# Optimization experiments

Measured on AMD Instinct MI355X. Metric: run time of the kernel, lower is better.

Reference implementation:

```python
import jax, jax.numpy as jnp
import numpy as np

B, N, DIM, H, DH = 4, 2048, 512, 8, 64  # patches_num == N (required by the math)
INNER = H * DH
SCALE = DH ** -0.5


def setup_inputs() -> dict:
    key = jax.random.key(0)
    ks = jax.random.split(key, 6)
    s = lambda fan_in: 1.0 / np.sqrt(fan_in)
    return {
        "x": jax.random.normal(ks[0], (B, N, DIM), dtype=jnp.float32),
        "w_qkfv": jax.random.normal(ks[1], (DIM, 4 * INNER), dtype=jnp.float32) * s(DIM),
        "w_scales": jax.random.normal(ks[2], (DH, N), dtype=jnp.float32) * s(DH),
        "b_scales": jax.random.normal(ks[3], (N,), dtype=jnp.float32) * s(DH),
        "w_out": jax.random.normal(ks[4], (INNER, DIM), dtype=jnp.float32) * s(INNER),
        "b_out": jax.random.normal(ks[5], (DIM,), dtype=jnp.float32) * s(INNER),
    }


def reference(x, w_qkfv, w_scales, b_scales, w_out, b_out):
    # Fused qkfv projection: [B,N,4*INNER]
    qkfv = x @ w_qkfv
    q, k, f, v = jnp.split(qkfv, 4, axis=-1)
    split_heads = lambda t: t.reshape(B, N, H, DH).transpose(0, 2, 1, 3)  # b h n d
    q, k, f, v = map(split_heads, (q, k, f, v))

    # q @ k^T * scale -> [b,h,n,n]
    scores = jnp.einsum("bhid,bhjd->bhij", q, k) * SCALE
    attn = jax.nn.softmax(scores, axis=-1)

    # f^T @ v -> [b,h,d,d], then Linear(dim_head -> patches_num) -> [b,h,d,n]
    poss_value = jnp.einsum("bhnd,bhne->bhde", f, v)
    poss_value = poss_value @ w_scales + b_scales  # [b,h,d,n]

    # attn @ poss_value^T -> [b,h,n,d]
    out = jnp.einsum("bhij,bhdj->bhid", attn, poss_value)
    out = out.transpose(0, 2, 1, 3).reshape(B, N, INNER)  # b n (h d)

    # to_out (dropout=0 / eval mode -> identity)
    return out @ w_out + b_out
```

## Files before the change

### kernel.cpp

```cpp
#include <hip/hip_runtime.h>
#include <stdint.h>

#define N_SEQ 2048
#define QKFV_COLS 2048

typedef __attribute__((ext_vector_type(8))) __bf16 bf16x8;
typedef __attribute__((ext_vector_type(4))) __bf16 bf16x4;
typedef __attribute__((ext_vector_type(4))) float f32x4;
typedef __attribute__((ext_vector_type(16))) float f32x16;

#if __has_builtin(__builtin_amdgcn_exp2f)
#define EXP2(x) __builtin_amdgcn_exp2f(x)
#else
#define EXP2(x) exp2f(x)
#endif

__device__ __forceinline__ f32x4 mfma16(bf16x8 a, bf16x8 b, f32x4 c) {
  return __builtin_amdgcn_mfma_f32_16x16x32_bf16(a, b, c, 0, 0, 0);
}
__device__ __forceinline__ f32x16 mfma32(bf16x8 a, bf16x8 b, f32x16 c) {
  return __builtin_amdgcn_mfma_f32_32x32x16_bf16(a, b, c, 0, 0, 0);
}

__device__ __forceinline__ void glds16(const void* g, void* l) {
  __builtin_amdgcn_global_load_lds(
      (__attribute__((address_space(1))) uint32_t*)(uintptr_t)g,
      (__attribute__((address_space(3))) uint32_t*)l, 16, 0, 0);
}

__global__ __launch_bounds__(256) void prep_kernel(const float* __restrict__ wqk,
                                                   __bf16* __restrict__ wqT,
                                                   const float* __restrict__ wo,
                                                   __bf16* __restrict__ woT,
                                                   const float* __restrict__ wsc,
                                                   __bf16* __restrict__ wscT) {
  const int t = threadIdx.x;
  int bid = blockIdx.x;
  const float* in;
  __bf16* outp;
  int R, C, rt, ct;
  if (bid < 256) { in = wqk; outp = wqT; R = 512; C = 2048; rt = bid >> 5; ct = bid & 31; }
  else if (bid < 320) { int b2 = bid - 256; in = wo; outp = woT; R = 512; C = 512; rt = b2 >> 3; ct = b2 & 7; }
  else { int b2 = bid - 320; in = wsc; outp = wscT; R = 64; C = 2048; rt = 0; ct = b2; }
  __shared__ __bf16 tile[64][72];
  const int r0 = rt * 64, c0 = ct * 64;
  {
    const int r = t >> 2, cq = (t & 3) * 16;
    const float* src = in + (size_t)(r0 + r) * C + c0 + cq;
#pragma unroll
    for (int q = 0; q < 4; ++q) {
      f32x4 v = *(const f32x4*)(src + q * 4);
#pragma unroll
      for (int e = 0; e < 4; ++e) tile[r][cq + q * 4 + e] = (__bf16)v[e];
    }
  }
  __syncthreads();
  {
    const int c = t >> 2, rq = (t & 3) * 16;
    __bf16* dst = outp + (size_t)(c0 + c) * R + r0 + rq;
    bf16x8 o0, o1;
#pragma unroll
    for (int j = 0; j < 8; ++j) { o0[j] = tile[rq + j][c]; o1[j] = tile[rq + 8 + j][c]; }
    *(bf16x8*)dst = o0;
    *(bf16x8*)(dst + 8) = o1;
  }
}

__global__ __launch_bounds__(512, 4) void gemm_qkfv_kernel(const float* __restrict__ X,
                                                           const __bf16* __restrict__ Bt,
                                                           __bf16* __restrict__ C,
                                                           __bf16* __restrict__ fT,
                                                           __bf16* __restrict__ vT) {
  __shared__ alignas(16) __bf16 Ab[2][128 * 32];
  __shared__ alignas(16) __bf16 Bb[2][256 * 32];
  const int K = 512, N = 2048;
  const int t = threadIdx.x;
  const int w = t >> 6;
  const int lane = t & 63;
  const int l15 = lane & 15;
  const int q4 = lane >> 4;
  const int g4 = q4 * 4;
  const int wr = w >> 2, wc = w & 3;
  const int bid = blockIdx.x;
  const int n0 = (bid & 7) * 256;
  const int m0 = (bid >> 3) * 128;

  const float* srcAf;
  {
    int r = t >> 2, u = (t & 3) ^ (r & 3);
    srcAf = X + (size_t)(m0 + r) * K + u * 8;
  }
  const __bf16* srcB[2];
#pragma unroll
  for (int c = 0; c < 2; ++c) {
    int s = c * 512 + t, r = s >> 2, u = (s & 3) ^ (r & 3);
    srcB[c] = Bt + (size_t)(n0 + r) * K + u * 8;
  }

  f32x4 acc[4][4];
#pragma unroll
  for (int m = 0; m < 4; ++m)
#pragma unroll
    for (int n = 0; n < 4; ++n) acc[m][n] = (f32x4){0.f, 0.f, 0.f, 0.f};

  {
    f32x4 a0 = *(const f32x4*)(srcAf);
    f32x4 a1 = *(const f32x4*)(srcAf + 4);
    glds16(srcB[0], &Bb[0][t * 8]);
    glds16(srcB[1], &Bb[0][(512 + t) * 8]);
    bf16x8 aw;
#pragma unroll
    for (int e = 0; e < 4; ++e) { aw[e] = (__bf16)a0[e]; aw[4 + e] = (__bf16)a1[e]; }
    *(bf16x8*)&Ab[0][t * 8] = aw;
  }

  for (int kt = 0; kt < 16; ++kt) {
    const int cur = kt & 1;
    asm volatile("s_waitcnt vmcnt(0) lgkmcnt(0)" ::: "memory");
    __builtin_amdgcn_s_barrier();
    f32x4 a0, a1;
    const bool pf = kt < 15;
    if (pf) {
      const int k0 = (kt + 1) * 32;
      a0 = *(const f32x4*)(srcAf + k0);
      a1 = *(const f32x4*)(srcAf + k0 + 4);
      glds16(srcB[0] + k0, &Bb[cur ^ 1][t * 8]);
      glds16(srcB[1] + k0, &Bb[cur ^ 1][(512 + t) * 8]);
    }
    bf16x8 af[4], bf[4];
#pragma unroll
    for (int m = 0; m < 4; ++m) {
      const int R = wr * 64 + m * 16 + l15;
      af[m] = *(const bf16x8*)&Ab[cur][R * 32 + ((q4 ^ (R & 3)) * 8)];
    }
#pragma unroll
    for (int n = 0; n < 4; ++n) {
      const int R = wc * 64 + n * 16 + l15;
      bf[n] = *(const bf16x8*)&Bb[cur][R * 32 + ((q4 ^ (R & 3)) * 8)];
    }
    __builtin_amdgcn_s_setprio(1);
#pragma unroll
    for (int m = 0; m < 4; ++m)
#pragma unroll
      for (int n = 0; n < 4; ++n) acc[m][n] = mfma16(af[m], bf[n], acc[m][n]);
    __builtin_amdgcn_s_setprio(0);
    if (pf) {
      bf16x8 aw;
#pragma unroll
      for (int e = 0; e < 4; ++e) { aw[e] = (__bf16)a0[e]; aw[4 + e] = (__bf16)a1[e]; }
      *(bf16x8*)&Ab[cur ^ 1][t * 8] = aw;
    }
    __builtin_amdgcn_s_barrier();
  }

  if (n0 < 1024) {
#pragma unroll
    for (int m = 0; m < 4; ++m)
#pragma unroll
      for (int n = 0; n < 4; ++n) {
        const int col = n0 + wc * 64 + n * 16 + l15;
        const int row = m0 + wr * 64 + m * 16 + g4;
#pragma unroll
        for (int r = 0; r < 4; ++r)
          C[(size_t)(row + r) * N + col] = (__bf16)acc[m][n][r];
      }
  } else {
    __bf16* T = (n0 < 1536) ? fT : vT;
    const int cbase = (n0 < 1536) ? 1024 : 1536;
#pragma unroll
    for (int m = 0; m < 4; ++m)
#pragma unroll
      for (int n = 0; n < 4; ++n) {
        const int hc = n0 + wc * 64 + n * 16 + l15 - cbase;
        const int h = hc >> 6, d = hc & 63;
        const int row = m0 + wr * 64 + m * 16 + g4;
        const int b = row >> 11, nl = row & 2047;
        bf16x4 pk;
#pragma unroll
        for (int r = 0; r < 4; ++r) pk[r] = (__bf16)acc[m][n][r];
        *(bf16x4*)&T[(size_t)((b * 8 + h) * 64 + d) * 2048 + nl] = pk;
      }
  }
}

__global__ __launch_bounds__(512, 4) void gemm_out_kernel(const __bf16* __restrict__ A,
                                                          const __bf16* __restrict__ Bt,
                                                          float* __restrict__ out,
                                                          const float* __restrict__ bias) {
  __shared__ alignas(16) __bf16 Ab[2][128 * 32];
  __shared__ alignas(16) __bf16 Bb[2][64 * 32];
  const int K = 512, N = 512;
  const int t = threadIdx.x;
  const int w = t >> 6;
  const int lane = t & 63;
  const int l15 = lane & 15;
  const int q4 = lane >> 4;
  const int g4 = q4 * 4;
  const int wr = w >> 1, wc = w & 1;
  const int bid = blockIdx.x;
  const int m0 = (((bid & 7) | (((bid >> 3) & 7) << 3))) * 128;
  const int n0 = (bid >> 6) * 64;

  const __bf16* srcA;
  const __bf16* srcB;
  {
    int s = t, r = s >> 2, u = (s & 3) ^ (r & 3);
    srcA = A + (size_t)(m0 + r) * K + u * 8;
    srcB = Bt + (size_t)(n0 + (r & 63)) * K + u * 8;
  }

  f32x4 acc[2][2];
#pragma unroll
  for (int m = 0; m < 2; ++m)
#pragma unroll
    for (int n = 0; n < 2; ++n) acc[m][n] = (f32x4){0.f, 0.f, 0.f, 0.f};

  glds16(srcA, &Ab[0][t * 8]);
  if (t < 256) glds16(srcB, &Bb[0][t * 8]);

  for (int kt = 0; kt < 16; ++kt) {
    const int cur = kt & 1;
    asm volatile("s_waitcnt vmcnt(0)" ::: "memory");
    __builtin_amdgcn_s_barrier();
    if (kt < 15) {
      const int k0 = (kt + 1) * 32;
      glds16(srcA + k0, &Ab[cur ^ 1][t * 8]);
      if (t < 256) glds16(srcB + k0, &Bb[cur ^ 1][t * 8]);
    }
    bf16x8 af[2], bf[2];
#pragma unroll
    for (int m = 0; m < 2; ++m) {
      const int R = wr * 32 + m * 16 + l15;
      af[m] = *(const bf16x8*)&Ab[cur][R * 32 + ((q4 ^ (R & 3)) * 8)];
    }
#pragma unroll
    for (int n = 0; n < 2; ++n) {
      const int R = wc * 32 + n * 16 + l15;
      bf[n] = *(const bf16x8*)&Bb[cur][R * 32 + ((q4 ^ (R & 3)) * 8)];
    }
    __builtin_amdgcn_s_setprio(1);
#pragma unroll
    for (int m = 0; m < 2; ++m)
#pragma unroll
      for (int n = 0; n < 2; ++n) acc[m][n] = mfma16(af[m], bf[n], acc[m][n]);
    __builtin_amdgcn_s_setprio(0);
    __builtin_amdgcn_s_barrier();
  }

#pragma unroll
  for (int m = 0; m < 2; ++m)
#pragma unroll
    for (int n = 0; n < 2; ++n) {
      const int col = n0 + wc * 32 + n * 16 + l15;
      const float bv = bias[col];
      const int row = m0 + wr * 32 + m * 16 + g4;
#pragma unroll
      for (int r = 0; r < 4; ++r)
        out[(size_t)(row + r) * N + col] = acc[m][n][r] + bv;
    }
}

__global__ __launch_bounds__(256) void fvmm_kernel(const __bf16* __restrict__ fT,
                                                   const __bf16* __restrict__ vT,
                                                   float* __restrict__ fvp) {
  __shared__ alignas(16) __bf16 As[2 * 8192];
  __shared__ alignas(16) __bf16 Bs[2 * 8192];
  const int t = threadIdx.x;
  const int w = t >> 6;
  const int lane = t & 63;
  const int l15 = lane & 15;
  const int q4 = lane >> 4;
  const int g4 = q4 * 4;
  const int sl = blockIdx.x;
  const int bh = blockIdx.y;
  const int k0 = sl * 256;
  const __bf16* A = fT + (size_t)bh * 131072 + k0;
  const __bf16* B = vT + (size_t)bh * 131072 + k0;

#pragma unroll
  for (int kt = 0; kt < 2; ++kt)
#pragma unroll
    for (int c = 0; c < 4; ++c) {
      int slot = c * 256 + t;
      int r = slot >> 4, u = (slot & 15) ^ (r & 7);
      glds16(A + (size_t)r * 2048 + kt * 128 + u * 8, &As[kt * 8192 + (c * 256 + w * 64) * 8]);
      glds16(B + (size_t)r * 2048 + kt * 128 + u * 8, &Bs[kt * 8192 + (c * 256 + w * 64) * 8]);
    }
  asm volatile("s_waitcnt vmcnt(0)" ::: "memory");
  __syncthreads();

  f32x4 acc[4];
#pragma unroll
  for (int nb = 0; nb < 4; ++nb) acc[nb] = (f32x4){0.f, 0.f, 0.f, 0.f};
  const int arow = w * 16 + l15;
#pragma unroll
  for (int ks = 0; ks < 8; ++ks) {
    const int kt = ks >> 2;
    const int ku = (ks & 3) * 4 + q4;
    bf16x8 a = *(const bf16x8*)&As[kt * 8192 + arow * 128 + ((ku ^ (arow & 7)) * 8)];
#pragma unroll
    for (int nb = 0; nb < 4; ++nb) {
      const int br = nb * 16 + l15;
      bf16x8 bb = *(const bf16x8*)&Bs[kt * 8192 + br * 128 + ((ku ^ (br & 7)) * 8)];
      acc[nb] = mfma16(a, bb, acc[nb]);
    }
  }
  float* dst = fvp + (size_t)(sl * 32 + bh) * 4096;
#pragma unroll
  for (int nb = 0; nb < 4; ++nb)
#pragma unroll
    for (int r = 0; r < 4; ++r)
      dst[(w * 16 + g4 + r) * 64 + nb * 16 + l15] = acc[nb][r];
}

__global__ __launch_bounds__(256) void pvmat2_kernel(const float* __restrict__ fvp,
                                                     const __bf16* __restrict__ wscT,
                                                     const float* __restrict__ bsc,
                                                     __bf16* __restrict__ pvm) {
  __shared__ alignas(16) __bf16 fs[64 * 72];
  __shared__ alignas(16) __bf16 Ws[128 * 64];
  const int t = threadIdx.x;
  const int w = t >> 6;
  const int lane = t & 63;
  const int l15 = lane & 15;
  const int q4 = lane >> 4;
  const int g4 = q4 * 4;
  const int bh = blockIdx.y;
  const int j0 = blockIdx.x * 128;

#pragma unroll
  for (int c = 0; c < 4; ++c) {
    int slot = c * 256 + t;
    int r = slot >> 3, u = (slot & 7) ^ (r & 7);
    glds16(wscT + (size_t)(j0 + r) * 64 + u * 8, &Ws[(c * 256 + w * 64) * 8]);
  }
#pragma unroll
  for (int qq = 0; qq < 4; ++qq) {
    int idx = t * 16 + qq * 4;
    f32x4 s = (f32x4){0.f, 0.f, 0.f, 0.f};
#pragma unroll
    for (int sl = 0; sl < 8; ++sl)
      s += *(const f32x4*)&fvp[(size_t)(sl * 32 + bh) * 4096 + idx];
    bf16x4 pk;
#pragma unroll
    for (int e = 0; e < 4; ++e) pk[e] = (__bf16)s[e];
    *(bf16x4*)&fs[(idx >> 6) * 72 + (idx & 63)] = pk;
  }
  asm volatile("s_waitcnt vmcnt(0)" ::: "memory");
  __syncthreads();

  f32x4 acc[8];
#pragma unroll
  for (int nb = 0; nb < 8; ++nb) {
    float bv = bsc[j0 + nb * 16 + l15];
    acc[nb] = (f32x4){bv, bv, bv, bv};
  }
  const int arow = w * 16 + l15;
#pragma unroll
  for (int ks = 0; ks < 2; ++ks) {
    bf16x8 a = *(const bf16x8*)&fs[arow * 72 + ks * 32 + q4 * 8];
#pragma unroll
    for (int nb = 0; nb < 8; ++nb) {
      const int jr = nb * 16 + l15;
      bf16x8 bb = *(const bf16x8*)&Ws[jr * 64 + (((ks * 4 + q4) ^ (jr & 7)) * 8)];
      acc[nb] = mfma16(a, bb, acc[nb]);
    }
  }
  __bf16* dst = pvm + (size_t)bh * 131072 + (size_t)j0;
#pragma unroll
  for (int nb = 0; nb < 8; ++nb)
#pragma unroll
    for (int r = 0; r < 4; ++r)
      dst[(size_t)(w * 16 + g4 + r) * 2048 + nb * 16 + l15] = (__bf16)acc[nb][r];
}

__global__ __launch_bounds__(512, 4) void attn_kernel(const __bf16* __restrict__ qkfv,
                                                      const __bf16* __restrict__ pvm,
                                                      __bf16* __restrict__ obuf) {
  __shared__ alignas(16) char smem[65536];
  __bf16* Kb = (__bf16*)smem;
  __bf16* Vb = (__bf16*)(smem + 32768);
  const int t = threadIdx.x;
  const int w = t >> 6;
  const int g = w >> 2;
  const int wq = w & 3;
  const int lane = t & 63;
  const int ln = lane & 31;
  const int hi = lane >> 5;
  const int p = blockIdx.x;
  const int bh = (p & 7) * 4 + ((p >> 3) & 3);
  const int iblk = p >> 5;
  const int b = bh >> 3, h = bh & 7;
  const int irow = iblk * 128 + wq * 32 + ln;
  const float K1 = 0.18033688f;
  const int swz = ln & 7;

  bf16x8 q[4];
  const __bf16* qrow = qkfv + (size_t)(b * N_SEQ + irow) * QKFV_COLS + h * 64 + hi * 8;
#pragma unroll
  for (int kf = 0; kf < 4; ++kf) {
    bf16x8 raw = *(const bf16x8*)(qrow + kf * 16);
#pragma unroll
    for (int e = 0; e < 8; ++e) q[kf][e] = (__bf16)((float)raw[e] * K1);
  }

  const int tg = t & 255;
  const __bf16* ksrc[2];
  const __bf16* vsrc[2];
#pragma unroll
  for (int it = 0; it < 2; ++it) {
    int s = it * 256 + tg;
    int r = s >> 3;
    int u = (s & 7) ^ (r & 7);
    ksrc[it] = qkfv + (size_t)(b * N_SEQ + g * 1024 + r) * QKFV_COLS + 512 + h * 64 + u * 8;
    vsrc[it] = pvm + ((size_t)bh * 64 + r) * 2048 + g * 1024 + u * 8;
  }

  auto stage = [&](int buf, int jt) {
#pragma unroll
    for (int it = 0; it < 2; ++it) {
      glds16(ksrc[it] + ((size_t)jt << 17), &Kb[(g * 2 + buf) * 4096 + (it * 256 + wq * 64) * 8]);
      glds16(vsrc[it] + jt * 64, &Vb[(g * 2 + buf) * 4096 + (it * 256 + wq * 64) * 8]);
    }
  };

  f32x16 o0, o1;
#pragma unroll
  for (int e = 0; e < 16; ++e) { o0[e] = 0.f; o1[e] = 0.f; }
  float lrl = 0.f;

  stage(0, 0);

  for (int jt = 0; jt < 16; ++jt) {
    asm volatile("s_waitcnt vmcnt(0)" ::: "memory");
    __builtin_amdgcn_s_barrier();
    if (jt < 15) stage((jt & 1) ^ 1, jt + 1);
    const int kc = (g * 2 + (jt & 1)) * 4096;

    f32x16 s0, s1;
#pragma unroll
    for (int e = 0; e < 16; ++e) { s0[e] = 0.f; s1[e] = 0.f; }
    __builtin_amdgcn_s_setprio(1);
#pragma unroll
    for (int kf = 0; kf < 4; ++kf) {
      bf16x8 k0 = *(const bf16x8*)&Kb[kc + (ln) * 64 + (((2 * kf + hi) ^ swz) * 8)];
      bf16x8 k1 = *(const bf16x8*)&Kb[kc + (32 + ln) * 64 + (((2 * kf + hi) ^ swz) * 8)];
      s0 = mfma32(k0, q[kf], s0);
      s1 = mfma32(k1, q[kf], s1);
    }
    __builtin_amdgcn_s_setprio(0);

#pragma unroll
    for (int e = 0; e < 16; ++e) s0[e] = EXP2(s0[e]);
#pragma unroll
    for (int e = 0; e < 16; ++e) s1[e] = EXP2(s1[e]);
    float a8[8];
#pragma unroll
    for (int e = 0; e < 8; ++e)
      a8[e] = (s0[e] + s0[e + 8]) + (s1[e] + s1[e + 8]);
    lrl += ((a8[0] + a8[4]) + (a8[1] + a8[5])) + ((a8[2] + a8[6]) + (a8[3] + a8[7]));

    bf16x8 pa[4];
#pragma unroll
    for (int kk = 0; kk < 4; ++kk) {
      const f32x16& sf = (kk < 2) ? s0 : s1;
      const int rb = (kk & 1) * 8;
      uint32_t a0, a1, b0, b1;
      asm("v_cvt_pk_bf16_f32 %0, %1, %2" : "=v"(a0) : "v"(sf[rb + 0]), "v"(sf[rb + 1]));
      asm("v_cvt_pk_bf16_f32 %0, %1, %2" : "=v"(a1) : "v"(sf[rb + 2]), "v"(sf[rb + 3]));
      asm("v_cvt_pk_bf16_f32 %0, %1, %2" : "=v"(b0) : "v"(sf[rb + 4]), "v"(sf[rb + 5]));
      asm("v_cvt_pk_bf16_f32 %0, %1, %2" : "=v"(b1) : "v"(sf[rb + 6]), "v"(sf[rb + 7]));
      asm("v_permlane32_swap_b32 %0, %1" : "+v"(a0), "+v"(b0));
      asm("v_permlane32_swap_b32 %0, %1" : "+v"(a1), "+v"(b1));
      union { uint32_t u[4]; bf16x8 v; } cv;
      cv.u[0] = a0; cv.u[1] = a1; cv.u[2] = b0; cv.u[3] = b1;
      pa[kk] = cv.v;
    }

    __builtin_amdgcn_s_setprio(1);
#pragma unroll
    for (int kk = 0; kk < 4; ++kk) {
      bf16x8 v0 = *(const bf16x8*)&Vb[kc + (ln) * 64 + (((2 * kk + hi) ^ swz) * 8)];
      bf16x8 v1 = *(const bf16x8*)&Vb[kc + (32 + ln) * 64 + (((2 * kk + hi) ^ swz) * 8)];
      o0 = mfma32(v0, pa[kk], o0);
      o1 = mfma32(v1, pa[kk], o1);
    }
    __builtin_amdgcn_s_setprio(0);
  }

  lrl += __shfl_xor(lrl, 32);

  __syncthreads();
  float* Om = (float*)smem;
  if (w >= 4) {
    const int base = ((w - 4) * 64 + lane) * 33;
#pragma unroll
    for (int e = 0; e < 16; ++e) { Om[base + e] = o0[e]; Om[base + 16 + e] = o1[e]; }
    Om[base + 32] = lrl;
  }
  __syncthreads();
  if (w < 4) {
    const int base = (w * 64 + lane) * 33;
#pragma unroll
    for (int e = 0; e < 16; ++e) { o0[e] += Om[base + e]; o1[e] += Om[base + 16 + e]; }
    lrl += Om[base + 32];

    const float inv = 1.0f / lrl;
    const size_t orow = (size_t)(b * N_SEQ + irow) * 512 + h * 64;
#pragma unroll
    for (int df = 0; df < 2; ++df) {
      const f32x16& oo = df ? o1 : o0;
#pragma unroll
      for (int gg = 0; gg < 4; ++gg) {
        bf16x4 pk;
#pragma unroll
        for (int e = 0; e < 4; ++e) pk[e] = (__bf16)(oo[gg * 4 + e] * inv);
        *(bf16x4*)(obuf + orow + df * 32 + gg * 8 + hi * 4) = pk;
      }
    }
  }
}

extern "C" void kernel_launch(void* const* d_in, const int* in_sizes, int n_in,
                              void* d_out, int out_size, void* d_ws, size_t ws_size,
                              hipStream_t stream) {
  (void)in_sizes; (void)n_in; (void)out_size; (void)ws_size;
  const float* x   = (const float*)d_in[0];
  const float* wqk = (const float*)d_in[1];
  const float* wsc = (const float*)d_in[2];
  const float* bsc = (const float*)d_in[3];
  const float* wo  = (const float*)d_in[4];
  const float* bo  = (const float*)d_in[5];
  float* out = (float*)d_out;

  char* p = (char*)d_ws;
  float*  fvp  = (float*)p;   p += (size_t)8192 * 512 * 2;
  __bf16* wqT  = (__bf16*)p;  p += (size_t)2048 * 512 * 2;
  __bf16* woT  = (__bf16*)p;  p += (size_t)512 * 512 * 2;
  __bf16* wscT = (__bf16*)p;  p += (size_t)2048 * 64 * 2;
  __bf16* qkfv = (__bf16*)p;  p += (size_t)8192 * 2048 * 2;
  __bf16* pvm  = (__bf16*)p;  p += (size_t)32 * 64 * 2048 * 2;
  __bf16* obuf = (__bf16*)p;  p += (size_t)8192 * 512 * 2;
  __bf16* fT = obuf;
  __bf16* vT = pvm;

  prep_kernel<<<dim3(352), dim3(256), 0, stream>>>(wqk, wqT, wo, woT, wsc, wscT);
  gemm_qkfv_kernel<<<dim3(512), dim3(512), 0, stream>>>(x, wqT, qkfv, fT, vT);
  fvmm_kernel<<<dim3(8, 32), dim3(256), 0, stream>>>(fT, vT, fvp);
  pvmat2_kernel<<<dim3(16, 32), dim3(256), 0, stream>>>(fvp, wscT, bsc, pvm);
  attn_kernel<<<dim3(512), dim3(512), 0, stream>>>(qkfv, pvm, obuf);
  gemm_out_kernel<<<dim3(512), dim3(512), 0, stream>>>(obuf, woT, out, bo);
}
```

Measured before the change: 112.0 us.

## Pre-swizzle poss_value into MFMA fragment layout and load it directly to registers

```diff
diff --git a/kernel.cpp b/kernel.cpp
--- a/kernel.cpp
+++ b/kernel.cpp
@@ -366,20 +366,30 @@
       acc[nb] = mfma16(a, bb, acc[nb]);
     }
   }
-  __bf16* dst = pvm + (size_t)bh * 131072 + (size_t)j0;
-#pragma unroll
-  for (int nb = 0; nb < 8; ++nb)
-#pragma unroll
-    for (int r = 0; r < 4; ++r)
-      dst[(size_t)(w * 16 + g4 + r) * 2048 + nb * 16 + l15] = (__bf16)acc[nb][r];
-}
-
-__global__ __launch_bounds__(512, 4) void attn_kernel(const __bf16* __restrict__ qkfv,
-                                                      const __bf16* __restrict__ pvm,
-                                                      __bf16* __restrict__ obuf) {
-  __shared__ alignas(16) char smem[65536];
+  __bf16* dst = pvm + (size_t)bh * 131072;
+  const int jtb = blockIdx.x * 2;
+  const int hi2 = l15 >> 3;
+  const int e = l15 & 7;
+#pragma unroll
+  for (int nb = 0; nb < 8; ++nb) {
+    const int jt = jtb + (nb >> 2);
+    const int kk = nb & 3;
+#pragma unroll
+    for (int r = 0; r < 4; ++r) {
+      const int d = w * 16 + g4 + r;
+      const int dblk = d >> 5, ln2 = d & 31;
+      dst[(size_t)(jt * 8 + dblk * 4 + kk) * 512 + hi2 * 256 + ln2 * 8 + e] = (__bf16)acc[nb][r];
+    }
+  }
+}
+
+__global__ __launch_bounds__(512)
+__attribute__((amdgpu_waves_per_eu(4, 4)))
+void attn_kernel(const __bf16* __restrict__ qkfv,
+                 const __bf16* __restrict__ pvm,
+                 __bf16* __restrict__ obuf) {
+  __shared__ alignas(16) char smem[36864];
   __bf16* Kb = (__bf16*)smem;
-  __bf16* Vb = (__bf16*)(smem + 32768);
   const int t = threadIdx.x;
   const int w = t >> 6;
   const int g = w >> 2;
@@ -406,22 +416,19 @@
 
   const int tg = t & 255;
   const __bf16* ksrc[2];
-  const __bf16* vsrc[2];
 #pragma unroll
   for (int it = 0; it < 2; ++it) {
     int s = it * 256 + tg;
     int r = s >> 3;
     int u = (s & 7) ^ (r & 7);
     ksrc[it] = qkfv + (size_t)(b * N_SEQ + g * 1024 + r) * QKFV_COLS + 512 + h * 64 + u * 8;
-    vsrc[it] = pvm + ((size_t)bh * 64 + r) * 2048 + g * 1024 + u * 8;
-  }
+  }
+  const __bf16* vbase = pvm + (size_t)bh * 131072 + lane * 8;
 
   auto stage = [&](int buf, int jt) {
 #pragma unroll
-    for (int it = 0; it < 2; ++it) {
+    for (int it = 0; it < 2; ++it)
       glds16(ksrc[it] + ((size_t)jt << 17), &Kb[(g * 2 + buf) * 4096 + (it * 256 + wq * 64) * 8]);
-      glds16(vsrc[it] + jt * 64, &Vb[(g * 2 + buf) * 4096 + (it * 256 + wq * 64) * 8]);
-    }
   };
 
   f32x16 o0, o1;
@@ -436,6 +443,14 @@
     __builtin_amdgcn_s_barrier();
     if (jt < 15) stage((jt & 1) ^ 1, jt + 1);
     const int kc = (g * 2 + (jt & 1)) * 4096;
+    const int jtg = g * 16 + jt;
+
+    bf16x8 vf0[4], vf1[4];
+#pragma unroll
+    for (int kk = 0; kk < 4; ++kk) {
+      vf0[kk] = *(const bf16x8*)(vbase + (size_t)(jtg * 8 + kk) * 512);
+      vf1[kk] = *(const bf16x8*)(vbase + (size_t)(jtg * 8 + 4 + kk) * 512);
+    }
 
     f32x16 s0, s1;
 #pragma unroll
@@ -480,10 +495,8 @@
     __builtin_amdgcn_s_setprio(1);
 #pragma unroll
     for (int kk = 0; kk < 4; ++kk) {
-      bf16x8 v0 = *(const bf16x8*)&Vb[kc + (ln) * 64 + (((2 * kk + hi) ^ swz) * 8)];
-      bf16x8 v1 = *(const bf16x8*)&Vb[kc + (32 + ln) * 64 + (((2 * kk + hi) ^ swz) * 8)];
-      o0 = mfma32(v0, pa[kk], o0);
-      o1 = mfma32(v1, pa[kk], o1);
+      o0 = mfma32(vf0[kk], pa[kk], o0);
+      o1 = mfma32(vf1[kk], pa[kk], o1);
     }
     __builtin_amdgcn_s_setprio(0);
   }
```

After: 151.0 us. 1.35x slower.
